# Performance work log

Measured on AMD Instinct MI355X. Metric: run time of the kernel, lower is better.

## Reference

```python
import jax, jax.numpy as jnp
import numpy as np

D_MODEL = 1024
NUM_HEADS = 16
D_K = D_MODEL // NUM_HEADS


def setup_inputs() -> dict:
    key = jax.random.key(0)
    ks = jax.random.split(key, 9)
    B, S = 4, 2048
    scale = 1.0 / np.sqrt(D_MODEL)
    return {
        "hidden_states": jax.random.normal(ks[0], (B, S, D_MODEL), dtype=jnp.float32),
        "Wq": jax.random.normal(ks[1], (D_MODEL, D_MODEL), dtype=jnp.float32) * scale,
        "bq": jax.random.normal(ks[2], (D_MODEL,), dtype=jnp.float32) * 0.02,
        "Wk": jax.random.normal(ks[3], (D_MODEL, D_MODEL), dtype=jnp.float32) * scale,
        "bk": jax.random.normal(ks[4], (D_MODEL,), dtype=jnp.float32) * 0.02,
        "Wv": jax.random.normal(ks[5], (D_MODEL, D_MODEL), dtype=jnp.float32) * scale,
        "bv": jax.random.normal(ks[6], (D_MODEL,), dtype=jnp.float32) * 0.02,
        "Wout": jax.random.normal(ks[7], (D_MODEL, D_MODEL), dtype=jnp.float32) * scale,
        "bout": jax.random.normal(ks[8], (D_MODEL,), dtype=jnp.float32) * 0.02,
    }


def _split_heads(x):
    # [B, S, D] -> [B, H, S, d_k]
    B, S, _ = x.shape
    return x.reshape(B, S, NUM_HEADS, D_K).transpose(0, 2, 1, 3)


def reference(hidden_states, Wq, bq, Wk, bk, Wv, bv, Wout, bout):
    # torch nn.Linear convention: y = x @ W.T + b
    q = _split_heads(hidden_states @ Wq.T + bq)
    k = _split_heads(hidden_states @ Wk.T + bk)
    v = _split_heads(hidden_states @ Wv.T + bv)
    # scaled dot-product attention (no mask, matching attention_mask=None)
    scores = jnp.einsum("bhqd,bhkd->bhqk", q, k) / jnp.sqrt(jnp.float32(D_K))
    attn = jax.nn.softmax(scores, axis=-1)
    ctx = jnp.einsum("bhqk,bhkd->bhqd", attn, v)
    # concatenate heads: [B, H, S, d_k] -> [B, S, D]
    B, H, S, dk = ctx.shape
    ctx = ctx.transpose(0, 2, 1, 3).reshape(B, S, H * dk)
    return ctx @ Wout.T + bout
```

## Files before the change

### kernel.cpp

```cpp
#include <hip/hip_runtime.h>
#include <hip/hip_bf16.h>
#include <stdint.h>

#define DEV_INLINE __device__ __forceinline__

typedef __attribute__((ext_vector_type(4))) float f32x4;
typedef __attribute__((ext_vector_type(16))) float f32x16;
typedef __attribute__((ext_vector_type(8))) short short8;
typedef __attribute__((ext_vector_type(2))) unsigned uint2v;

static constexpr int S_LEN = 2048;
static constexpr int DM = 1024;
static constexpr int NH = 16;
static constexpr int DK = 64;
static constexpr int BATCH = 4;
static constexpr int M_TOT = BATCH * S_LEN;

#define QSCALE 0.18033688011112042f

DEV_INLINE unsigned short bf_round(float x) {
  unsigned u = __builtin_bit_cast(unsigned, x);
  u += 0x7fffu + ((u >> 16) & 1u);
  return (unsigned short)(u >> 16);
}

struct CvtArgs {
  const float* in[5];
  unsigned short* out[5];
};
__global__ __launch_bounds__(256) void cvt_all(CvtArgs a) {
  int bid = blockIdx.x;
  int which, base;
  if (bid < 4096) { which = 0; base = bid; }
  else { int r = bid - 4096; which = 1 + (r >> 9); base = r & 511; }
  const float* __restrict__ in = a.in[which];
  unsigned short* __restrict__ out = a.out[which];
  long i = ((long)base * 256 + threadIdx.x) * 8;
  float4 va = *reinterpret_cast<const float4*>(in + i);
  float4 vb = *reinterpret_cast<const float4*>(in + i + 4);
  union { unsigned short u[8]; uint4 v; } pk;
  pk.u[0] = bf_round(va.x); pk.u[1] = bf_round(va.y);
  pk.u[2] = bf_round(va.z); pk.u[3] = bf_round(va.w);
  pk.u[4] = bf_round(vb.x); pk.u[5] = bf_round(vb.y);
  pk.u[6] = bf_round(vb.z); pk.u[7] = bf_round(vb.w);
  *reinterpret_cast<uint4*>(out + i) = pk.v;
}

DEV_INLINE void gload_lds16(const unsigned short* g, unsigned short* l) {
  __builtin_amdgcn_global_load_lds(
      (const __attribute__((address_space(1))) unsigned int*)g,
      (__attribute__((address_space(3))) unsigned int*)l,
      16, 0, 0);
}

DEV_INLINE void gemm_swz(int lin, int& bm, int& bn) {
  const int xcd = lin & 7, j = (lin >> 3) & 7;
  bm = xcd * 8 + j;
  bn = lin >> 6;
}

struct QkvArgs {
  const unsigned short* W[3];
  const float* bias[3];
  unsigned short* out[3];
};
__global__ __launch_bounds__(256) void gemm_qkv(const unsigned short* __restrict__ A,
                                                QkvArgs args) {
  constexpr int K = DM;
  __shared__ unsigned short lA[128 * 32];
  __shared__ unsigned short lB[128 * 32];
  const int tid = threadIdx.x;
  const int wave = tid >> 6, lane = tid & 63;
  const int wm = wave >> 1, wn = wave & 1;
  const int g = lane >> 4, c = lane & 15;
  int bm, bn;
  gemm_swz(blockIdx.y * 64 + blockIdx.x, bm, bn);
  const int z = blockIdx.z;

  const unsigned short* __restrict__ W = args.W[z];
  const float* __restrict__ bias = args.bias[z];
  unsigned short* __restrict__ outp = args.out[z];

  const int srow = lane >> 2;
  const int scol = (lane & 3) * 8;

  f32x4 acc[4][4] = {};

  const unsigned short* Abase = A + (long)(bm * 128) * K;
  const unsigned short* Wbase = W + (long)(bn * 128) * K;

  for (int k0 = 0; k0 < K; k0 += 32) {
    __syncthreads();
#pragma unroll
    for (int i = 0; i < 2; ++i) {
      const int row = i * 64 + wave * 16;
      gload_lds16(Abase + (long)(row + srow) * K + k0 + scol, lA + row * 32);
      gload_lds16(Wbase + (long)(row + srow) * K + k0 + scol, lB + row * 32);
    }
    __syncthreads();

    short8 af[4], bf[4];
#pragma unroll
    for (int mi = 0; mi < 4; ++mi)
      af[mi] = *reinterpret_cast<const short8*>(&lA[(wm * 64 + mi * 16 + c) * 32 + g * 8]);
#pragma unroll
    for (int ni = 0; ni < 4; ++ni)
      bf[ni] = *reinterpret_cast<const short8*>(&lB[(wn * 64 + ni * 16 + c) * 32 + g * 8]);
#pragma unroll
    for (int mi = 0; mi < 4; ++mi)
#pragma unroll
      for (int ni = 0; ni < 4; ++ni)
        acc[mi][ni] =
            __builtin_amdgcn_mfma_f32_16x16x32_bf16(af[mi], bf[ni], acc[mi][ni], 0, 0, 0);
  }

#pragma unroll
  for (int mi = 0; mi < 4; ++mi) {
#pragma unroll
    for (int ni = 0; ni < 4; ++ni) {
      const int mg0 = bm * 128 + wm * 64 + mi * 16 + g * 4;
      const int ng = bn * 128 + wn * 64 + ni * 16 + c;
      const float bv = bias[ng];
#pragma unroll
      for (int r = 0; r < 4; ++r) {
        const int m = mg0 + r;
        float v = acc[mi][ni][r] + bv;
        if (z == 0) v *= QSCALE;
        const int b_ = m >> 11, s_ = m & 2047, h_ = ng >> 6, d_ = ng & 63;
        if (z < 2) {
          outp[((long)(b_ * NH + h_) * S_LEN + s_) * DK + d_] = bf_round(v);
        } else {
          outp[((long)(b_ * NH + h_) * DK + d_) * S_LEN + s_] = bf_round(v);
        }
      }
    }
  }
}

__global__ __launch_bounds__(256) void gemm_out(const unsigned short* __restrict__ A,
                                                const unsigned short* __restrict__ W,
                                                const float* __restrict__ bias,
                                                float* __restrict__ outp) {
  constexpr int K = DM, N = DM;
  __shared__ unsigned short lA[128 * 32];
  __shared__ unsigned short lB[128 * 32];
  const int tid = threadIdx.x;
  const int wave = tid >> 6, lane = tid & 63;
  const int wm = wave >> 1, wn = wave & 1;
  const int g = lane >> 4, c = lane & 15;
  int bm, bn;
  gemm_swz(blockIdx.y * 64 + blockIdx.x, bm, bn);

  const int srow = lane >> 2;
  const int scol = (lane & 3) * 8;

  f32x4 acc[4][4] = {};

  const unsigned short* Abase = A + (long)(bm * 128) * K;
  const unsigned short* Wbase = W + (long)(bn * 128) * K;

  for (int k0 = 0; k0 < K; k0 += 32) {
    __syncthreads();
#pragma unroll
    for (int i = 0; i < 2; ++i) {
      const int row = i * 64 + wave * 16;
      gload_lds16(Abase + (long)(row + srow) * K + k0 + scol, lA + row * 32);
      gload_lds16(Wbase + (long)(row + srow) * K + k0 + scol, lB + row * 32);
    }
    __syncthreads();

    short8 af[4], bf[4];
#pragma unroll
    for (int mi = 0; mi < 4; ++mi)
      af[mi] = *reinterpret_cast<const short8*>(&lA[(wm * 64 + mi * 16 + c) * 32 + g * 8]);
#pragma unroll
    for (int ni = 0; ni < 4; ++ni)
      bf[ni] = *reinterpret_cast<const short8*>(&lB[(wn * 64 + ni * 16 + c) * 32 + g * 8]);
#pragma unroll
    for (int mi = 0; mi < 4; ++mi)
#pragma unroll
      for (int ni = 0; ni < 4; ++ni)
        acc[mi][ni] =
            __builtin_amdgcn_mfma_f32_16x16x32_bf16(af[mi], bf[ni], acc[mi][ni], 0, 0, 0);
  }

#pragma unroll
  for (int mi = 0; mi < 4; ++mi) {
#pragma unroll
    for (int ni = 0; ni < 4; ++ni) {
      const int mg0 = bm * 128 + wm * 64 + mi * 16 + g * 4;
      const int ng = bn * 128 + wn * 64 + ni * 16 + c;
      const float bv = bias[ng];
#pragma unroll
      for (int r = 0; r < 4; ++r)
        outp[(long)(mg0 + r) * N + ng] = acc[mi][ni][r] + bv;
    }
  }
}

__global__ __launch_bounds__(256) void attn_kernel(const unsigned short* __restrict__ Q,
                                                   const unsigned short* __restrict__ Kb,
                                                   const unsigned short* __restrict__ Vt,
                                                   unsigned short* __restrict__ ctx) {
  __shared__ unsigned short kbuf[2][2][64 * 64];
  __shared__ unsigned short vbuf[2][2][64 * 64];
  const int tid = threadIdx.x, wave = tid >> 6, lane = tid & 63;
  const int q = lane & 31;
  const int h = lane >> 5;
  const int bid = blockIdx.x;
  const int swz = (bid & 7) * 128 + (bid >> 3);
  const int hd = swz >> 4, qb = swz & 15;
  const int q0 = qb * 128 + wave * 32;

  const unsigned short* Qh = Q + (long)hd * S_LEN * DK;
  const char* KhB = (const char*)(Kb + (long)hd * S_LEN * DK);
  const char* VhB = (const char*)(Vt + (long)hd * DK * S_LEN);

  const int srow_in = lane >> 3;
  const int scolb = ((lane & 7) * 16) ^ (srow_in << 4);

  auto ldsrd = [&](const unsigned short* buf, int row, int colbyte) -> short8 {
    return *reinterpret_cast<const short8*>(
        reinterpret_cast<const char*>(buf) + row * 128 + (colbyte ^ ((row & 7) << 4)));
  };

  auto stage = [&](int b, int kv0) {
#pragma unroll
    for (int sub = 0; sub < 2; ++sub) {
#pragma unroll
      for (int r = 0; r < 2; ++r) {
        const int rowbase = (wave * 2 + r) * 8;
        const int row = rowbase + srow_in;
        gload_lds16((const unsigned short*)(KhB + (long)(kv0 + sub * 64 + row) * 128 + scolb),
                    &kbuf[b][sub][rowbase * 64]);
        gload_lds16((const unsigned short*)(VhB + (long)row * (S_LEN * 2) +
                                            (kv0 + sub * 64) * 2 + scolb),
                    &vbuf[b][sub][rowbase * 64]);
      }
    }
  };

  short8 qf[4];
#pragma unroll
  for (int d0 = 0; d0 < 4; ++d0)
    qf[d0] = *reinterpret_cast<const short8*>(&Qh[(long)(q0 + q) * DK + d0 * 16 + h * 8]);

  union { short s[8]; short8 v; } ones_u;
#pragma unroll
  for (int i = 0; i < 8; ++i) ones_u.s[i] = (short)0x3F80;
  const short8 ones8 = ones_u.v;

  f32x16 cacc0 = {}, cacc1 = {};
  f32x16 lacc = {};
  float mrun = -1e30f;

  stage(0, 0);
  __syncthreads();

  int cur = 0;
  for (int t = 0; t < S_LEN / 128; ++t) {
    if (t + 1 < S_LEN / 128) stage(cur ^ 1, (t + 1) * 128);

#pragma unroll
    for (int p = 0; p < 2; ++p) {
      const unsigned short* kb = kbuf[cur][p];
      const unsigned short* vb = vbuf[cur][p];

      short8 kfA[4], kfB[4];
#pragma unroll
      for (int d0 = 0; d0 < 4; ++d0) {
        kfA[d0] = ldsrd(kb, q, d0 * 32 + h * 16);
        kfB[d0] = ldsrd(kb, 32 + q, d0 * 32 + h * 16);
      }
      __builtin_amdgcn_s_setprio(1);
      f32x16 stA = {}, stB = {};
#pragma unroll
      for (int d0 = 0; d0 < 4; ++d0) {
        stA = __builtin_amdgcn_mfma_f32_32x32x16_bf16(kfA[d0], qf[d0], stA, 0, 0, 0);
        stB = __builtin_amdgcn_mfma_f32_32x32x16_bf16(kfB[d0], qf[d0], stB, 0, 0, 0);
      }
      __builtin_amdgcn_s_setprio(0);

      float m0 = fmaxf(fmaxf(stA[0], stA[1]), stA[2]);
      float m1 = fmaxf(fmaxf(stA[3], stA[4]), stA[5]);
      float m2 = fmaxf(fmaxf(stA[6], stA[7]), stA[8]);
      float m3 = fmaxf(fmaxf(stA[9], stA[10]), stA[11]);
      float m4 = fmaxf(fmaxf(stA[12], stA[13]), stA[14]);
      float m5 = fmaxf(fmaxf(stA[15], stB[0]), stB[1]);
      float m6 = fmaxf(fmaxf(stB[2], stB[3]), stB[4]);
      float m7 = fmaxf(fmaxf(stB[5], stB[6]), stB[7]);
      float m8 = fmaxf(fmaxf(stB[8], stB[9]), stB[10]);
      float m9 = fmaxf(fmaxf(stB[11], stB[12]), stB[13]);
      float n0 = fmaxf(fmaxf(m0, m1), m2);
      float n1 = fmaxf(fmaxf(m3, m4), m5);
      float n2 = fmaxf(fmaxf(m6, m7), m8);
      float n3 = fmaxf(fmaxf(m9, stB[14]), stB[15]);
      const float pml = fmaxf(fmaxf(n0, n1), fmaxf(n2, n3));

      if (__any(pml > mrun + 8.0f)) {
        const float pm = fmaxf(pml, __shfl_xor(pml, 32));
        const float mnew = fmaxf(mrun, pm);
        const float alpha = __builtin_amdgcn_exp2f(mrun - mnew);
        cacc0 *= alpha;
        cacc1 *= alpha;
        lacc *= alpha;
        mrun = mnew;
      }

#pragma unroll
      for (int r = 0; r < 16; ++r) {
        stA[r] = __builtin_amdgcn_exp2f(stA[r] - mrun);
        stB[r] = __builtin_amdgcn_exp2f(stB[r] - mrun);
      }

      unsigned pAA[4], pAB[4], pBA[4], pBB[4];
#pragma unroll
      for (int rq = 0; rq < 4; ++rq) {
        asm("v_cvt_pk_bf16_f32 %0, %1, %2" : "=v"(pAA[rq]) : "v"(stA[4 * rq]), "v"(stA[4 * rq + 1]));
        asm("v_cvt_pk_bf16_f32 %0, %1, %2" : "=v"(pAB[rq]) : "v"(stA[4 * rq + 2]), "v"(stA[4 * rq + 3]));
        asm("v_cvt_pk_bf16_f32 %0, %1, %2" : "=v"(pBA[rq]) : "v"(stB[4 * rq]), "v"(stB[4 * rq + 1]));
        asm("v_cvt_pk_bf16_f32 %0, %1, %2" : "=v"(pBB[rq]) : "v"(stB[4 * rq + 2]), "v"(stB[4 * rq + 3]));
      }

      short8 vf0[4], vf1[4];
#pragma unroll
      for (int s = 0; s < 4; ++s) {
        vf0[s] = ldsrd(vb, q, s * 32 + h * 16);
        vf1[s] = ldsrd(vb, 32 + q, s * 32 + h * 16);
      }
      __builtin_amdgcn_s_setprio(1);
#pragma unroll
      for (int s = 0; s < 4; ++s) {
        const unsigned a0 = (s < 2 ? pAA : pBA)[2 * (s & 1)];
        const unsigned a1 = (s < 2 ? pAA : pBA)[2 * (s & 1) + 1];
        const unsigned b0 = (s < 2 ? pAB : pBB)[2 * (s & 1)];
        const unsigned b1 = (s < 2 ? pAB : pBB)[2 * (s & 1) + 1];
        uint2v prA = __builtin_amdgcn_permlane32_swap(a0, a1, false, false);
        uint2v prB = __builtin_amdgcn_permlane32_swap(b0, b1, false, false);
        union { unsigned w[4]; short8 v; } pf;
        pf.w[0] = prA[0];
        pf.w[1] = prB[0];
        pf.w[2] = prA[1];
        pf.w[3] = prB[1];
        cacc0 = __builtin_amdgcn_mfma_f32_32x32x16_bf16(vf0[s], pf.v, cacc0, 0, 0, 0);
        cacc1 = __builtin_amdgcn_mfma_f32_32x32x16_bf16(vf1[s], pf.v, cacc1, 0, 0, 0);
        lacc = __builtin_amdgcn_mfma_f32_32x32x16_bf16(ones8, pf.v, lacc, 0, 0, 0);
      }
      __builtin_amdgcn_s_setprio(0);
    }

    __syncthreads();
    cur ^= 1;
  }

  const float inv = 1.0f / lacc[0];
  const int b_ = hd >> 4, h_ = hd & 15;
  const long row = ((long)b_ * S_LEN + q0 + q) * DM + h_ * DK;
#pragma unroll
  for (int rq = 0; rq < 4; ++rq) {
    ushort4 w0, w1;
    w0.x = bf_round(cacc0[4 * rq + 0] * inv);
    w0.y = bf_round(cacc0[4 * rq + 1] * inv);
    w0.z = bf_round(cacc0[4 * rq + 2] * inv);
    w0.w = bf_round(cacc0[4 * rq + 3] * inv);
    w1.x = bf_round(cacc1[4 * rq + 0] * inv);
    w1.y = bf_round(cacc1[4 * rq + 1] * inv);
    w1.z = bf_round(cacc1[4 * rq + 2] * inv);
    w1.w = bf_round(cacc1[4 * rq + 3] * inv);
    *reinterpret_cast<ushort4*>(&ctx[row + 8 * rq + 4 * h]) = w0;
    *reinterpret_cast<ushort4*>(&ctx[row + 32 + 8 * rq + 4 * h]) = w1;
  }
}

extern "C" void kernel_launch(void* const* d_in, const int* in_sizes, int n_in,
                              void* d_out, int out_size, void* d_ws, size_t ws_size,
                              hipStream_t stream) {
  const float* X  = (const float*)d_in[0];
  const float* Wq = (const float*)d_in[1];
  const float* bq = (const float*)d_in[2];
  const float* Wk = (const float*)d_in[3];
  const float* bk = (const float*)d_in[4];
  const float* Wv = (const float*)d_in[5];
  const float* bv = (const float*)d_in[6];
  const float* Wo = (const float*)d_in[7];
  const float* bo = (const float*)d_in[8];

  char* ws = (char*)d_ws;
  const long MB = 1l << 20;
  unsigned short* Xbf = (unsigned short*)(ws + 0 * MB);
  unsigned short* Ctx = Xbf;
  unsigned short* Wqb = (unsigned short*)(ws + 16 * MB);
  unsigned short* Wkb = (unsigned short*)(ws + 18 * MB);
  unsigned short* Wvb = (unsigned short*)(ws + 20 * MB);
  unsigned short* Wob = (unsigned short*)(ws + 22 * MB);
  unsigned short* Qb  = (unsigned short*)(ws + 24 * MB);
  unsigned short* Kbf = (unsigned short*)(ws + 40 * MB);
  unsigned short* Vtb = (unsigned short*)(ws + 56 * MB);

  CvtArgs ca;
  ca.in[0] = X;  ca.out[0] = Xbf;
  ca.in[1] = Wq; ca.out[1] = Wqb;
  ca.in[2] = Wk; ca.out[2] = Wkb;
  ca.in[3] = Wv; ca.out[3] = Wvb;
  ca.in[4] = Wo; ca.out[4] = Wob;
  cvt_all<<<4096 + 4 * 512, 256, 0, stream>>>(ca);

  QkvArgs qa;
  qa.W[0] = Wqb; qa.bias[0] = bq; qa.out[0] = Qb;
  qa.W[1] = Wkb; qa.bias[1] = bk; qa.out[1] = Kbf;
  qa.W[2] = Wvb; qa.bias[2] = bv; qa.out[2] = Vtb;
  gemm_qkv<<<dim3(M_TOT / 128, DM / 128, 3), 256, 0, stream>>>(Xbf, qa);

  attn_kernel<<<dim3(1024), 256, 0, stream>>>(Qb, Kbf, Vtb, Ctx);

  gemm_out<<<dim3(M_TOT / 128, DM / 128), 256, 0, stream>>>(Ctx, Wob, bo, (float*)d_out);
}
```

Before: 216.7 us.

## Double GEMM K-tile to 64 with XOR-swizzled LDS and widen conversion per thread

Both projection GEMMs now stage 64-wide K slices instead of 32, which halves the number of barrier pairs per tile. The LDS layout uses an XOR swizzle on 16-byte chunks, applied to both the global_load_lds source addresses and the fragment reads, to avoid bank conflicts on the 128-byte rows. The fp32-to-bf16 conversion kernel has each thread process 16 elements, so it launches half as many blocks. In exchange, LDS use per block doubles and register pressure rises from holding two sets of fragments.

```diff
diff --git a/kernel.cpp b/kernel.cpp
--- a/kernel.cpp
+++ b/kernel.cpp
@@ -31,19 +31,22 @@
 __global__ __launch_bounds__(256) void cvt_all(CvtArgs a) {
   int bid = blockIdx.x;
   int which, base;
-  if (bid < 4096) { which = 0; base = bid; }
-  else { int r = bid - 4096; which = 1 + (r >> 9); base = r & 511; }
+  if (bid < 2048) { which = 0; base = bid; }
+  else { int r = bid - 2048; which = 1 + (r >> 8); base = r & 255; }
   const float* __restrict__ in = a.in[which];
   unsigned short* __restrict__ out = a.out[which];
-  long i = ((long)base * 256 + threadIdx.x) * 8;
-  float4 va = *reinterpret_cast<const float4*>(in + i);
-  float4 vb = *reinterpret_cast<const float4*>(in + i + 4);
-  union { unsigned short u[8]; uint4 v; } pk;
-  pk.u[0] = bf_round(va.x); pk.u[1] = bf_round(va.y);
-  pk.u[2] = bf_round(va.z); pk.u[3] = bf_round(va.w);
-  pk.u[4] = bf_round(vb.x); pk.u[5] = bf_round(vb.y);
-  pk.u[6] = bf_round(vb.z); pk.u[7] = bf_round(vb.w);
-  *reinterpret_cast<uint4*>(out + i) = pk.v;
+  long i = ((long)base * 256 + threadIdx.x) * 16;
+#pragma unroll
+  for (int half = 0; half < 2; ++half) {
+    float4 va = *reinterpret_cast<const float4*>(in + i + half * 8);
+    float4 vb = *reinterpret_cast<const float4*>(in + i + half * 8 + 4);
+    union { unsigned short u[8]; uint4 v; } pk;
+    pk.u[0] = bf_round(va.x); pk.u[1] = bf_round(va.y);
+    pk.u[2] = bf_round(va.z); pk.u[3] = bf_round(va.w);
+    pk.u[4] = bf_round(vb.x); pk.u[5] = bf_round(vb.y);
+    pk.u[6] = bf_round(vb.z); pk.u[7] = bf_round(vb.w);
+    *reinterpret_cast<uint4*>(out + i + half * 8) = pk.v;
+  }
 }
 
 DEV_INLINE void gload_lds16(const unsigned short* g, unsigned short* l) {
@@ -57,6 +60,11 @@
   const int xcd = lin & 7, j = (lin >> 3) & 7;
   bm = xcd * 8 + j;
   bn = lin >> 6;
+}
+
+DEV_INLINE short8 ldsrd128(const unsigned short* buf, int row, int colbyte) {
+  return *reinterpret_cast<const short8*>(
+      reinterpret_cast<const char*>(buf) + row * 128 + (colbyte ^ ((row & 7) << 4)));
 }
 
 struct QkvArgs {
@@ -67,8 +75,8 @@
 __global__ __launch_bounds__(256) void gemm_qkv(const unsigned short* __restrict__ A,
                                                 QkvArgs args) {
   constexpr int K = DM;
-  __shared__ unsigned short lA[128 * 32];
-  __shared__ unsigned short lB[128 * 32];
+  __shared__ unsigned short lA[128 * 64];
+  __shared__ unsigned short lB[128 * 64];
   const int tid = threadIdx.x;
   const int wave = tid >> 6, lane = tid & 63;
   const int wm = wave >> 1, wn = wave & 1;
@@ -81,37 +89,53 @@
   const float* __restrict__ bias = args.bias[z];
   unsigned short* __restrict__ outp = args.out[z];
 
-  const int srow = lane >> 2;
-  const int scol = (lane & 3) * 8;
+  const int srow_in = lane >> 3;
+  const int scolb = ((lane & 7) * 16) ^ (srow_in << 4);
 
   f32x4 acc[4][4] = {};
 
-  const unsigned short* Abase = A + (long)(bm * 128) * K;
-  const unsigned short* Wbase = W + (long)(bn * 128) * K;
-
-  for (int k0 = 0; k0 < K; k0 += 32) {
+  const char* AB = (const char*)A + (long)(bm * 128) * K * 2;
+  const char* WB = (const char*)W + (long)(bn * 128) * K * 2;
+
+  for (int k0 = 0; k0 < K; k0 += 64) {
     __syncthreads();
 #pragma unroll
-    for (int i = 0; i < 2; ++i) {
-      const int row = i * 64 + wave * 16;
-      gload_lds16(Abase + (long)(row + srow) * K + k0 + scol, lA + row * 32);
-      gload_lds16(Wbase + (long)(row + srow) * K + k0 + scol, lB + row * 32);
+    for (int j = 0; j < 4; ++j) {
+      const int rowbase = wave * 32 + j * 8;
+      gload_lds16((const unsigned short*)(AB + (long)(rowbase + srow_in) * (K * 2) +
+                                          k0 * 2 + scolb),
+                  lA + rowbase * 64);
+      gload_lds16((const unsigned short*)(WB + (long)(rowbase + srow_in) * (K * 2) +
+                                          k0 * 2 + scolb),
+                  lB + rowbase * 64);
     }
     __syncthreads();
 
-    short8 af[4], bf[4];
-#pragma unroll
-    for (int mi = 0; mi < 4; ++mi)
-      af[mi] = *reinterpret_cast<const short8*>(&lA[(wm * 64 + mi * 16 + c) * 32 + g * 8]);
-#pragma unroll
-    for (int ni = 0; ni < 4; ++ni)
-      bf[ni] = *reinterpret_cast<const short8*>(&lB[(wn * 64 + ni * 16 + c) * 32 + g * 8]);
+    short8 af0[4], af1[4], bf0[4], bf1[4];
+#pragma unroll
+    for (int mi = 0; mi < 4; ++mi) {
+      const int row = wm * 64 + mi * 16 + c;
+      af0[mi] = ldsrd128(lA, row, g * 16);
+      af1[mi] = ldsrd128(lA, row, 64 + g * 16);
+    }
+#pragma unroll
+    for (int ni = 0; ni < 4; ++ni) {
+      const int row = wn * 64 + ni * 16 + c;
+      bf0[ni] = ldsrd128(lB, row, g * 16);
+      bf1[ni] = ldsrd128(lB, row, 64 + g * 16);
+    }
 #pragma unroll
     for (int mi = 0; mi < 4; ++mi)
 #pragma unroll
       for (int ni = 0; ni < 4; ++ni)
         acc[mi][ni] =
-            __builtin_amdgcn_mfma_f32_16x16x32_bf16(af[mi], bf[ni], acc[mi][ni], 0, 0, 0);
+            __builtin_amdgcn_mfma_f32_16x16x32_bf16(af0[mi], bf0[ni], acc[mi][ni], 0, 0, 0);
+#pragma unroll
+    for (int mi = 0; mi < 4; ++mi)
+#pragma unroll
+      for (int ni = 0; ni < 4; ++ni)
+        acc[mi][ni] =
+            __builtin_amdgcn_mfma_f32_16x16x32_bf16(af1[mi], bf1[ni], acc[mi][ni], 0, 0, 0);
   }
 
 #pragma unroll
@@ -142,8 +166,8 @@
                                                 const float* __restrict__ bias,
                                                 float* __restrict__ outp) {
   constexpr int K = DM, N = DM;
-  __shared__ unsigned short lA[128 * 32];
-  __shared__ unsigned short lB[128 * 32];
+  __shared__ unsigned short lA[128 * 64];
+  __shared__ unsigned short lB[128 * 64];
   const int tid = threadIdx.x;
   const int wave = tid >> 6, lane = tid & 63;
   const int wm = wave >> 1, wn = wave & 1;
@@ -151,37 +175,53 @@
   int bm, bn;
   gemm_swz(blockIdx.y * 64 + blockIdx.x, bm, bn);
 
-  const int srow = lane >> 2;
-  const int scol = (lane & 3) * 8;
+  const int srow_in = lane >> 3;
+  const int scolb = ((lane & 7) * 16) ^ (srow_in << 4);
 
   f32x4 acc[4][4] = {};
 
-  const unsigned short* Abase = A + (long)(bm * 128) * K;
-  const unsigned short* Wbase = W + (long)(bn * 128) * K;
-
-  for (int k0 = 0; k0 < K; k0 += 32) {
+  const char* AB = (const char*)A + (long)(bm * 128) * K * 2;
+  const char* WB = (const char*)W + (long)(bn * 128) * K * 2;
+
+  for (int k0 = 0; k0 < K; k0 += 64) {
     __syncthreads();
 #pragma unroll
-    for (int i = 0; i < 2; ++i) {
-      const int row = i * 64 + wave * 16;
-      gload_lds16(Abase + (long)(row + srow) * K + k0 + scol, lA + row * 32);
-      gload_lds16(Wbase + (long)(row + srow) * K + k0 + scol, lB + row * 32);
+    for (int j = 0; j < 4; ++j) {
+      const int rowbase = wave * 32 + j * 8;
+      gload_lds16((const unsigned short*)(AB + (long)(rowbase + srow_in) * (K * 2) +
+                                          k0 * 2 + scolb),
+                  lA + rowbase * 64);
+      gload_lds16((const unsigned short*)(WB + (long)(rowbase + srow_in) * (K * 2) +
+                                          k0 * 2 + scolb),
+                  lB + rowbase * 64);
     }
     __syncthreads();
 
-    short8 af[4], bf[4];
-#pragma unroll
-    for (int mi = 0; mi < 4; ++mi)
-      af[mi] = *reinterpret_cast<const short8*>(&lA[(wm * 64 + mi * 16 + c) * 32 + g * 8]);
-#pragma unroll
-    for (int ni = 0; ni < 4; ++ni)
-      bf[ni] = *reinterpret_cast<const short8*>(&lB[(wn * 64 + ni * 16 + c) * 32 + g * 8]);
+    short8 af0[4], af1[4], bf0[4], bf1[4];
+#pragma unroll
+    for (int mi = 0; mi < 4; ++mi) {
+      const int row = wm * 64 + mi * 16 + c;
+      af0[mi] = ldsrd128(lA, row, g * 16);
+      af1[mi] = ldsrd128(lA, row, 64 + g * 16);
+    }
+#pragma unroll
+    for (int ni = 0; ni < 4; ++ni) {
+      const int row = wn * 64 + ni * 16 + c;
+      bf0[ni] = ldsrd128(lB, row, g * 16);
+      bf1[ni] = ldsrd128(lB, row, 64 + g * 16);
+    }
 #pragma unroll
     for (int mi = 0; mi < 4; ++mi)
 #pragma unroll
       for (int ni = 0; ni < 4; ++ni)
         acc[mi][ni] =
-            __builtin_amdgcn_mfma_f32_16x16x32_bf16(af[mi], bf[ni], acc[mi][ni], 0, 0, 0);
+            __builtin_amdgcn_mfma_f32_16x16x32_bf16(af0[mi], bf0[ni], acc[mi][ni], 0, 0, 0);
+#pragma unroll
+    for (int mi = 0; mi < 4; ++mi)
+#pragma unroll
+      for (int ni = 0; ni < 4; ++ni)
+        acc[mi][ni] =
+            __builtin_amdgcn_mfma_f32_16x16x32_bf16(af1[mi], bf1[ni], acc[mi][ni], 0, 0, 0);
   }
 
 #pragma unroll
@@ -403,7 +443,7 @@
   ca.in[2] = Wk; ca.out[2] = Wkb;
   ca.in[3] = Wv; ca.out[3] = Wvb;
   ca.in[4] = Wo; ca.out[4] = Wob;
-  cvt_all<<<4096 + 4 * 512, 256, 0, stream>>>(ca);
+  cvt_all<<<2048 + 4 * 256, 256, 0, stream>>>(ca);
 
   QkvArgs qa;
   qa.W[0] = Wqb; qa.bias[0] = bq; qa.out[0] = Qb;
```

Result: slower. 223.0 us (+2.9%).
